# Performance work log

Hardware: AMD Instinct MI355X
Metric: run time of the kernel (lower is better)

## Reference

```python
import jax, jax.numpy as jnp
import numpy as np

H = 16        # num attention heads
KVH = 4       # num key/value heads
D = 128       # head dim
WIN = 1024    # sliding window (in packed per-state positions)
THETA = 10000.0
NUM_STATES = 8


def rotate_half(x):
    half = x.shape[-1] // 2
    return jnp.concatenate([-x[..., half:], x[..., :half]], axis=-1)


def setup_inputs() -> dict:
    key = jax.random.key(0)
    ks = jax.random.split(key, 6)
    B, L, HID = 2, 2048, 2048
    s = 0.02
    hidden_states = jax.random.normal(ks[0], (B, L, HID), jnp.float32)
    Wq = jax.random.normal(ks[1], (H * D, HID), jnp.float32) * s
    Wk = jax.random.normal(ks[2], (KVH * D, HID), jnp.float32) * s
    Wv = jax.random.normal(ks[3], (KVH * D, HID), jnp.float32) * s
    Wo = jax.random.normal(ks[4], (HID, H * D), jnp.float32) * s
    sid = jax.random.randint(ks[5], (B, L), 0, NUM_STATES).astype(jnp.int64)
    position_ids = jnp.tile(jnp.arange(L, dtype=jnp.int64)[None, :], (B, 1))
    return dict(hidden_states=hidden_states, Wq=Wq, Wk=Wk, Wv=Wv, Wo=Wo,
                sid=sid, position_ids=position_ids)


def reference(hidden_states, Wq, Wk, Wv, Wo, sid, position_ids):
    B, L, HID = hidden_states.shape
    # projections (Linear without bias: x @ W.T)
    q = (hidden_states @ Wq.T).reshape(B, L, H, D)
    k = (hidden_states @ Wk.T).reshape(B, L, KVH, D)
    v = (hidden_states @ Wv.T).reshape(B, L, KVH, D)
    # rotary embedding
    inv_freq = 1.0 / (THETA ** (jnp.arange(0, D, 2, dtype=jnp.float32) / D))
    freqs = position_ids.astype(jnp.float32)[:, :, None] * inv_freq[None, None, :]  # [B,L,D/2]
    emb = jnp.concatenate([freqs, freqs], axis=-1)                                  # [B,L,D]
    cos = jnp.cos(emb)[:, :, None, :].astype(hidden_states.dtype)
    sin = jnp.sin(emb)[:, :, None, :].astype(hidden_states.dtype)
    q = q * cos + rotate_half(q) * sin
    k = k * cos + rotate_half(k) * sin
    # GQA: repeat kv heads (repeat_interleave along head dim)
    n_rep = H // KVH
    k = jnp.repeat(k, n_rep, axis=2)  # [B,L,H,D]
    v = jnp.repeat(v, n_rep, axis=2)
    # BoSs mask: attend within same state id, causal, sliding window over
    # packed-per-state rank distance (equivalent to the varlen packing path)
    same = sid[:, :, None] == sid[:, None, :]                  # [B,L,L]
    tril = jnp.tril(jnp.ones((L, L), dtype=bool))[None]        # [1,L,L]
    rank = jnp.sum(same & tril, axis=-1) - 1                   # [B,L] rank within own state
    win_ok = (rank[:, :, None] - rank[:, None, :]) <= WIN
    mask = same & tril & win_ok                                # [B,L,L]
    scale = D ** -0.5
    scores = jnp.einsum('bqhd,bkhd->bhqk', q, k) * scale       # [B,H,L,L]
    scores = jnp.where(mask[:, None, :, :], scores, jnp.finfo(scores.dtype).min)
    attn = jax.nn.softmax(scores, axis=-1)
    o = jnp.einsum('bhqk,bkhd->bqhd', attn, v).reshape(B, L, H * D)
    return o @ Wo.T
```

## Files before the change

kernel.cpp:

```cpp
#include <hip/hip_runtime.h>
#include <hip/hip_bf16.h>

#define H_ 16
#define KVH_ 4
#define D_ 128
#define L_ 2048
#define B_ 2
#define HID_ 2048
#define WIN_ 1024
#define NS_ 8
#define QKV_N 3072

typedef __attribute__((ext_vector_type(8))) short short8;
typedef __attribute__((ext_vector_type(4))) float floatx4;

__device__ inline float bf16_to_f(unsigned short u) {
    union { unsigned int i; float f; } c; c.i = ((unsigned int)u) << 16; return c.f;
}
__device__ inline unsigned short f_to_bf16(float f) {
    __hip_bfloat16 h = __float2bfloat16(f);
    return *(unsigned short*)&h;
}

__device__ inline int world_is_bf16(const unsigned short* hs_u) {
    int lane = threadIdx.x & 63;
    unsigned short u = hs_u[(lane & 31) * 2];
    int e = (u >> 7) & 0xFF;
    unsigned long long bad = __ballot(e > 130);
    return bad == 0ULL;
}
__device__ inline int pid_stride(const int* pids) { return (pids[1] == 0) ? 2 : 1; }

__global__ __launch_bounds__(256) void convert_all(const void* __restrict__ hs,
                                                   const void* __restrict__ Wq,
                                                   const void* __restrict__ Wk,
                                                   const void* __restrict__ Wv,
                                                   const void* __restrict__ Wo,
                                                   unsigned short* __restrict__ c_hs,
                                                   unsigned short* __restrict__ c_Wq,
                                                   unsigned short* __restrict__ c_Wk,
                                                   unsigned short* __restrict__ c_Wv,
                                                   unsigned short* __restrict__ c_Wo) {
    int isbf = world_is_bf16((const unsigned short*)hs);
    const int N0 = (B_ * L_ * HID_) / 4;
    const int N1 = (HID_ * HID_) / 4;
    const int N2 = (KVH_ * D_ * HID_) / 4;
    const int N3 = N2;
    const int N4 = N1;
    const int total = N0 + N1 + N2 + N3 + N4;
    for (int i = blockIdx.x * 256 + threadIdx.x; i < total; i += gridDim.x * 256) {
        int j = i;
        const void* src; unsigned short* dst;
        if (j < N0)              { src = hs; dst = c_hs; }
        else if ((j -= N0) < N1) { src = Wq; dst = c_Wq; }
        else if ((j -= N1) < N2) { src = Wk; dst = c_Wk; }
        else if ((j -= N2) < N3) { src = Wv; dst = c_Wv; }
        else                     { j -= N3; src = Wo; dst = c_Wo; }
        if (isbf) {
            ((ushort4*)dst)[j] = ((const ushort4*)src)[j];
        } else {
            float4 f = ((const float4*)src)[j];
            ushort4 o4;
            o4.x = f_to_bf16(f.x); o4.y = f_to_bf16(f.y);
            o4.z = f_to_bf16(f.z); o4.w = f_to_bf16(f.w);
            ((ushort4*)dst)[j] = o4;
        }
    }
}

__global__ __launch_bounds__(256) void scan_kernel(const int* __restrict__ sid,
                                                   const int* __restrict__ pids,
                                                   int* __restrict__ rank,
                                                   int* __restrict__ poslist,
                                                   int* __restrict__ counts) {
    int stride = pid_stride(pids);
    int b = blockIdx.x;
    int t = threadIdx.x;
    __shared__ int cnt[256][NS_];
    __shared__ int pre[256][NS_];
    const int* s = sid + (size_t)b * L_ * stride;
    int myid[8];
#pragma unroll
    for (int i = 0; i < 8; i++) myid[i] = s[(t * 8 + i) * stride];
#pragma unroll
    for (int st = 0; st < NS_; st++) cnt[t][st] = 0;
#pragma unroll
    for (int i = 0; i < 8; i++) cnt[t][myid[i]]++;
    __syncthreads();
    for (int off = 1; off < 256; off <<= 1) {
        int add[NS_];
        if (t >= off)
#pragma unroll
            for (int st = 0; st < NS_; st++) add[st] = cnt[t - off][st];
        __syncthreads();
        if (t >= off)
#pragma unroll
            for (int st = 0; st < NS_; st++) cnt[t][st] += add[st];
        __syncthreads();
    }
#pragma unroll
    for (int st = 0; st < NS_; st++) pre[t][st] = t ? cnt[t - 1][st] : 0;
    if (t == 255)
#pragma unroll
        for (int st = 0; st < NS_; st++) counts[b * NS_ + st] = cnt[255][st];
    __syncthreads();
#pragma unroll
    for (int i = 0; i < 8; i++) {
        int sd = myid[i];
        int r = pre[t][sd]++;
        int pos = t * 8 + i;
        rank[b * L_ + pos] = r;
        poslist[((size_t)b * NS_ + sd) * L_ + r] = pos;
    }
}

#define STAGE(gptr, ldsdst)                                                     \
    __builtin_amdgcn_global_load_lds(                                           \
        (const __attribute__((address_space(1))) unsigned int*)(gptr),          \
        (__attribute__((address_space(3))) unsigned int*)(ldsdst), 16, 0, 0)

#define SB __builtin_amdgcn_sched_barrier(0)

#define RD_A(dst, MH, KK)                                                       \
    _Pragma("unroll")                                                           \
    for (int mt = 0; mt < MT; ++mt)                                             \
        dst[mt] = *(const short8*)&Ab[(arow + (MH) * (MT * 16) + mt * 16) * 64  \
                                      + ((((KK) << 2) | quad) ^ axor) * 8]

#define RD_B(dst, KK)                                                           \
    _Pragma("unroll")                                                           \
    for (int nt = 0; nt < 4; ++nt)                                              \
        dst[nt] = *(const short8*)&Bb[(brr + nt * 16) * 64                      \
                                      + ((((KK) << 2) | quad) ^ axor) * 8]

#define MFMA_C(AV, BV, MH)                                                      \
    __builtin_amdgcn_s_setprio(1);                                              \
    _Pragma("unroll")                                                           \
    for (int mt = 0; mt < MT; ++mt)                                             \
        _Pragma("unroll")                                                       \
        for (int nt = 0; nt < 4; ++nt)                                          \
            acc[(MH) * MT + mt][nt] = __builtin_amdgcn_mfma_f32_16x16x32_bf16(  \
                AV[mt], BV[nt], acc[(MH) * MT + mt][nt], 0, 0, 0);              \
    __builtin_amdgcn_s_setprio(0)

template<int MT>
__global__ __launch_bounds__(512, 1) void gemm_t(const unsigned short* __restrict__ A,
                                                 const unsigned short* __restrict__ B0,
                                                 const unsigned short* __restrict__ B1,
                                                 const unsigned short* __restrict__ B2,
                                                 void* __restrict__ C,
                                                 int M, int N, int K,
                                                 int nb1, int nb2,
                                                 const unsigned short* __restrict__ hs_probe,
                                                 int c_mode) {
    __shared__ unsigned short As[2][MT * 4096];
    __shared__ unsigned short Bs[2][16384];
    int tid = threadIdx.x;
    int wave = tid >> 6, lane = tid & 63;
    int quad = lane >> 4, l16 = lane & 15;
    int wr = wave >> 2, wc = wave & 3;
    int bn_t = blockIdx.x;
    int bm = blockIdx.y * (MT * 64), bn = bn_t * 256;

    const unsigned short* Bseg;
    int brow0;
    if (bn_t < nb1)      { Bseg = B0; brow0 = bn; }
    else if (bn_t < nb2) { Bseg = B1; brow0 = bn - nb1 * 256; }
    else                 { Bseg = B2; brow0 = bn - nb2 * 256; }

    int sub = tid >> 3, slot = tid & 7;
    int swz = slot ^ (sub & 7);
    unsigned int a_off[MT], b_off[4];
#pragma unroll
    for (int c = 0; c < MT; ++c)
        a_off[c] = (unsigned int)((bm + c * 64 + sub) * K + swz * 8);
#pragma unroll
    for (int c = 0; c < 4; ++c)
        b_off[c] = (unsigned int)((brow0 + c * 64 + sub) * K + swz * 8);

    const int arow = wr * (MT * 32) + l16;
    const int brr  = wc * 64 + l16;
    const int axor = l16 & 7;

    floatx4 acc[2 * MT][4] = {};
    short8 a0[MT], a1[MT], b0[4], b1[4];
    const int KT = K >> 6;

#pragma unroll
    for (int c = 0; c < 4; ++c)  STAGE(Bseg + b_off[c], &Bs[0][c * 4096 + tid * 8]);
#pragma unroll
    for (int c = 0; c < MT; ++c) STAGE(A + a_off[c], &As[0][c * 4096 + tid * 8]);

    for (int t = 0; t < KT; ++t) {
        const unsigned short* Ab = As[t & 1];
        const unsigned short* Bb = Bs[t & 1];
        unsigned short* AsN = As[(t & 1) ^ 1];
        unsigned short* BsN = Bs[(t & 1) ^ 1];
        int tn = (t + 1 < KT) ? t + 1 : t;
        unsigned int kel = (unsigned int)tn * 64;

        asm volatile("s_waitcnt vmcnt(0)" ::: "memory");
        __builtin_amdgcn_s_barrier();
        asm volatile("" ::: "memory");

        RD_A(a0, 0, 0);
        RD_B(b0, 0);
        RD_A(a1, 1, 0);
#pragma unroll
        for (int c = 0; c < 4; ++c)
            STAGE(Bseg + b_off[c] + kel, &BsN[c * 4096 + tid * 8]);
        SB;
        MFMA_C(a0, b0, 0);
        SB;
        RD_A(a0, 0, 1);
        RD_B(b1, 1);
#pragma unroll
        for (int c = 0; c < MT; ++c)
            STAGE(A + a_off[c] + kel, &AsN[c * 4096 + tid * 8]);
        SB;
        MFMA_C(a1, b0, 1);
        SB;
        RD_A(a1, 1, 1);
        SB;
        MFMA_C(a0, b1, 0);
        SB;
        MFMA_C(a1, b1, 1);
    }
    asm volatile("s_waitcnt vmcnt(0)" ::: "memory");

    int cf32 = c_mode ? !world_is_bf16(hs_probe) : 0;
#pragma unroll
    for (int a = 0; a < 2 * MT; ++a)
#pragma unroll
        for (int g = 0; g < 4; ++g)
#pragma unroll
            for (int r = 0; r < 4; ++r) {
                int row = bm + wr * (MT * 32) + (a / MT) * (MT * 16)
                        + (a % MT) * 16 + quad * 4 + r;
                int col = bn + wc * 64 + g * 16 + l16;
                size_t idx = (size_t)row * N + col;
                if (cf32) ((float*)C)[idx] = acc[a][g][r];
                else      ((unsigned short*)C)[idx] = f_to_bf16(acc[a][g][r]);
            }
}

__global__ __launch_bounds__(256) void rope_kernel(unsigned short* __restrict__ qkv,
                                                   const int* __restrict__ pos_ids) {
    int stride = pid_stride(pos_ids);
    int idx = blockIdx.x * 256 + threadIdx.x;
    int i = idx & 63;
    int tmp = idx >> 6;
    int head = tmp % 20;
    int bl = tmp / 20;
    if (bl >= B_ * L_) return;
    float posf = (float)pos_ids[bl * stride];
    float inv = exp2f(-(float)i * (2.0f / 128.0f) * 13.287712379549449f);
    float ang = posf * inv;
    float c = cosf(ang), sn = sinf(ang);
    unsigned short* p = qkv + (size_t)bl * QKV_N +
                        ((head < H_) ? head * D_ : 2048 + (head - H_) * D_);
    float x0 = bf16_to_f(p[i]), x1 = bf16_to_f(p[i + 64]);
    p[i]      = f_to_bf16(x0 * c - x1 * sn);
    p[i + 64] = f_to_bf16(x1 * c + x0 * sn);
}

__global__ __launch_bounds__(256, 4) void attn_mfma(const unsigned short* __restrict__ qkv,
                                                    const int* __restrict__ counts,
                                                    const int* __restrict__ poslist,
                                                    unsigned short* __restrict__ o) {
    int qt  = blockIdx.x & 127;
    int kvh = (blockIdx.x >> 7) & 3;
    int s   = (blockIdx.x >> 9) & 7;
    int b   = blockIdx.x >> 12;
    int n = counts[b * NS_ + s];
    if (qt * 16 >= n) return;
    const int* plist = poslist + ((size_t)b * NS_ + s) * L_;

    __shared__ short Ksh[32][136];
    __shared__ short Vsh[128][40];
    __shared__ short Psh[4][16][40];
    __shared__ int posq[16];

    int tid = threadIdx.x;
    int wave = tid >> 6, lane = tid & 63;
    int quad = lane >> 4, l16 = lane & 15;
    int h = kvh * 4 + wave;
    const float scale = 0.08838834764831845f;

    if (tid < 16) posq[tid] = plist[min(qt * 16 + tid, n - 1)];
    __syncthreads();

    short8 qf[4];
    {
        const unsigned short* gq =
            qkv + ((size_t)(b << 11) + posq[l16]) * QKV_N + h * D_;
#pragma unroll
        for (int kk = 0; kk < 4; kk++)
            qf[kk] = *(const short8*)(gq + kk * 32 + quad * 8);
    }

    float m_r[4], l_r[4];
    floatx4 Ov[8];
#pragma unroll
    for (int r4 = 0; r4 < 4; r4++) { m_r[r4] = -1e30f; l_r[r4] = 0.f; }
#pragma unroll
    for (int nt = 0; nt < 8; nt++) Ov[nt] = (floatx4){0.f, 0.f, 0.f, 0.f};

    int c0 = max(0, (qt * 16 - WIN_) >> 5);
    int nch = ((qt * 16 + 15) >> 5) + 1;

    int r = tid >> 3, seg = tid & 7;
    int vc = r ^ ((seg & 3) << 3);
    short8 kr0, kr1, vr0, vr1;
    {
        int kpos = plist[min(c0 * 32 + r, n - 1)];
        size_t base = ((size_t)(b << 11) + kpos) * QKV_N + 2048 + kvh * D_ + seg * 16;
        kr0 = *(const short8*)(qkv + base);
        kr1 = *(const short8*)(qkv + base + 8);
        vr0 = *(const short8*)(qkv + base + 512);
        vr1 = *(const short8*)(qkv + base + 520);
    }

    for (int c = c0; c < nch; c++) {
        *(short8*)&Ksh[r][seg * 16]     = kr0;
        *(short8*)&Ksh[r][seg * 16 + 8] = kr1;
#pragma unroll
        for (int e = 0; e < 8; e++) Vsh[seg * 16 + e][vc] = vr0[e];
#pragma unroll
        for (int e = 0; e < 8; e++) Vsh[seg * 16 + 8 + e][vc] = vr1[e];
        __syncthreads();

        if (c + 1 < nch) {
            int kpos = plist[min((c + 1) * 32 + r, n - 1)];
            size_t base = ((size_t)(b << 11) + kpos) * QKV_N + 2048 + kvh * D_ + seg * 16;
            kr0 = *(const short8*)(qkv + base);
            kr1 = *(const short8*)(qkv + base + 8);
            vr0 = *(const short8*)(qkv + base + 512);
            vr1 = *(const short8*)(qkv + base + 520);
        }

        floatx4 s0 = (floatx4){0.f, 0.f, 0.f, 0.f};
        floatx4 s1 = (floatx4){0.f, 0.f, 0.f, 0.f};
#pragma unroll
        for (int kk = 0; kk < 4; kk++) {
            short8 kfa = *(const short8*)&Ksh[l16][kk * 32 + quad * 8];
            s0 = __builtin_amdgcn_mfma_f32_16x16x32_bf16(qf[kk], kfa, s0, 0, 0, 0);
        }
#pragma unroll
        for (int kk = 0; kk < 4; kk++) {
            short8 kfb = *(const short8*)&Ksh[16 + l16][kk * 32 + quad * 8];
            s1 = __builtin_amdgcn_mfma_f32_16x16x32_bf16(qf[kk], kfb, s1, 0, 0, 0);
        }

        int kr0i = c * 32 + l16, kr1i = kr0i + 16;
        float x0[4], x1[4], rmax[4];
#pragma unroll
        for (int r4 = 0; r4 < 4; r4++) {
            int qr = qt * 16 + quad * 4 + r4;
            bool mk0 = (kr0i <= qr) && (kr0i >= qr - WIN_);
            bool mk1 = (kr1i <= qr) && (kr1i >= qr - WIN_);
            x0[r4] = mk0 ? s0[r4] * scale : -1e30f;
            x1[r4] = mk1 ? s1[r4] * scale : -1e30f;
            rmax[r4] = fmaxf(x0[r4], x1[r4]);
        }
#pragma unroll
        for (int st = 1; st <= 8; st <<= 1)
#pragma unroll
            for (int r4 = 0; r4 < 4; r4++)
                rmax[r4] = fmaxf(rmax[r4], __shfl_xor(rmax[r4], st, 64));
        float al[4], psum[4];
#pragma unroll
        for (int r4 = 0; r4 < 4; r4++) {
            float nm = fmaxf(m_r[r4], rmax[r4]);
            al[r4] = __expf(m_r[r4] - nm);
            m_r[r4] = nm;
            x0[r4] = (x0[r4] > -1e29f) ? __expf(x0[r4] - nm) : 0.f;
            x1[r4] = (x1[r4] > -1e29f) ? __expf(x1[r4] - nm) : 0.f;
            psum[r4] = x0[r4] + x1[r4];
        }
#pragma unroll
        for (int st = 1; st <= 8; st <<= 1)
#pragma unroll
            for (int r4 = 0; r4 < 4; r4++)
                psum[r4] += __shfl_xor(psum[r4], st, 64);
#pragma unroll
        for (int r4 = 0; r4 < 4; r4++) l_r[r4] = l_r[r4] * al[r4] + psum[r4];
#pragma unroll
        for (int nt = 0; nt < 8; nt++)
#pragma unroll
            for (int r4 = 0; r4 < 4; r4++) Ov[nt][r4] *= al[r4];

#pragma unroll
        for (int r4 = 0; r4 < 4; r4++) {
            Psh[wave][quad * 4 + r4][l16]      = (short)f_to_bf16(x0[r4]);
            Psh[wave][quad * 4 + r4][16 + l16] = (short)f_to_bf16(x1[r4]);
        }
        short8 pf = *(const short8*)&Psh[wave][l16][quad * 8];

#pragma unroll
        for (int nt = 0; nt < 8; nt++) {
            short8 vf = *(const short8*)&Vsh[nt * 16 + l16][(quad ^ (nt & 3)) * 8];
            Ov[nt] = __builtin_amdgcn_mfma_f32_16x16x32_bf16(pf, vf, Ov[nt], 0, 0, 0);
        }
        __syncthreads();
    }

    float inv_r[4];
    int pos_r[4], qvalid[4];
#pragma unroll
    for (int r4 = 0; r4 < 4; r4++) {
        int qr = qt * 16 + quad * 4 + r4;
        qvalid[r4] = (qr < n);
        inv_r[r4] = 1.f / l_r[r4];
        pos_r[r4] = posq[quad * 4 + r4];
    }
#pragma unroll
    for (int nt = 0; nt < 8; nt++)
#pragma unroll
        for (int r4 = 0; r4 < 4; r4++)
            if (qvalid[r4])
                o[(((size_t)(b << 11) + pos_r[r4]) * H_ + h) * D_ + nt * 16 + l16] =
                    f_to_bf16(Ov[nt][r4] * inv_r[r4]);
}

extern "C" void kernel_launch(void* const* d_in, const int* in_sizes, int n_in,
                              void* d_out, int out_size, void* d_ws, size_t ws_size,
                              hipStream_t stream) {
    const void* hs = d_in[0];
    const void* Wq = d_in[1];
    const void* Wk = d_in[2];
    const void* Wv = d_in[3];
    const void* Wo = d_in[4];
    const int* sid  = (const int*)d_in[5];
    const int* pids = (const int*)d_in[6];

    const int M = B_ * L_;
    char* w = (char*)d_ws;
    unsigned short* qkv  = (unsigned short*)(w + 256);
    unsigned short* o_b  = (unsigned short*)(w + 25166080);
    unsigned short* c_hs = (unsigned short*)(w + 41943296);
    unsigned short* c_Wq = (unsigned short*)(w + 58720512);
    unsigned short* c_Wk = (unsigned short*)(w + 67109120);
    unsigned short* c_Wv = (unsigned short*)(w + 69206272);
    unsigned short* c_Wo = (unsigned short*)(w + 71303424);
    int* rank            = (int*)(w + 79692032);
    int* plist           = (int*)(w + 79708416);
    int* counts          = (int*)(w + 79839488);

    const unsigned short* hs_probe = (const unsigned short*)hs;

    convert_all<<<2048, 256, 0, stream>>>(hs, Wq, Wk, Wv, Wo,
                                          c_hs, c_Wq, c_Wk, c_Wv, c_Wo);

    scan_kernel<<<B_, 256, 0, stream>>>(sid, pids, rank, plist, counts);

    gemm_t<4><<<dim3(QKV_N / 256, M / 256), 512, 0, stream>>>(
        c_hs, c_Wq, c_Wk, c_Wv, qkv, M, QKV_N, HID_, 8, 10, hs_probe, 0);

    int rope_threads = M * (H_ + KVH_) * 64;
    rope_kernel<<<(rope_threads + 255) / 256, 256, 0, stream>>>(qkv, pids);

    attn_mfma<<<B_ * NS_ * KVH_ * (L_ / 16), 256, 0, stream>>>(qkv, counts, plist, o_b);

    gemm_t<2><<<dim3(HID_ / 256, M / 128), 512, 0, stream>>>(
        o_b, c_Wo, c_Wo, c_Wo, d_out, M, HID_, HID_, 1 << 30, 1 << 30, hs_probe, 1);
}
```

Before: 300.3 us.

## Deepen GEMM pipeline to four-stage LDS ring with K=32 tiles

The projection GEMM's K-step shrinks from 64 to 32, and the double-buffered LDS is replaced by a 4-slot ring with 3 tiles prefetched ahead. The full vmcnt(0) wait becomes a partial vmcnt wait, so loads stay in flight across iterations. The LDS swizzle changes to a 4-slot XOR pattern and all fragments are read up front before the MFMAs. The aim is to hide global latency better, at the cost of twice as many barriers per K and a different bank-conflict pattern.

```diff
diff --git a/kernel.cpp b/kernel.cpp
--- a/kernel.cpp
+++ b/kernel.cpp
@@ -121,26 +121,14 @@
 
 #define SB __builtin_amdgcn_sched_barrier(0)
 
-#define RD_A(dst, MH, KK)                                                       \
-    _Pragma("unroll")                                                           \
-    for (int mt = 0; mt < MT; ++mt)                                             \
-        dst[mt] = *(const short8*)&Ab[(arow + (MH) * (MT * 16) + mt * 16) * 64  \
-                                      + ((((KK) << 2) | quad) ^ axor) * 8]
-
-#define RD_B(dst, KK)                                                           \
-    _Pragma("unroll")                                                           \
-    for (int nt = 0; nt < 4; ++nt)                                              \
-        dst[nt] = *(const short8*)&Bb[(brr + nt * 16) * 64                      \
-                                      + ((((KK) << 2) | quad) ^ axor) * 8]
-
-#define MFMA_C(AV, BV, MH)                                                      \
+#define MFMA_P(P)                                                               \
     __builtin_amdgcn_s_setprio(1);                                              \
     _Pragma("unroll")                                                           \
-    for (int mt = 0; mt < MT; ++mt)                                             \
+    for (int m2 = 0; m2 < 2; ++m2)                                              \
         _Pragma("unroll")                                                       \
         for (int nt = 0; nt < 4; ++nt)                                          \
-            acc[(MH) * MT + mt][nt] = __builtin_amdgcn_mfma_f32_16x16x32_bf16(  \
-                AV[mt], BV[nt], acc[(MH) * MT + mt][nt], 0, 0, 0);              \
+            acc[(P) * 2 + m2][nt] = __builtin_amdgcn_mfma_f32_16x16x32_bf16(    \
+                fA[(P) * 2 + m2], fB[nt], acc[(P) * 2 + m2][nt], 0, 0, 0);      \
     __builtin_amdgcn_s_setprio(0)
 
 template<int MT>
@@ -153,8 +141,9 @@
                                                  int nb1, int nb2,
                                                  const unsigned short* __restrict__ hs_probe,
                                                  int c_mode) {
-    __shared__ unsigned short As[2][MT * 4096];
-    __shared__ unsigned short Bs[2][16384];
+    const int CH_A = MT / 2;
+    __shared__ unsigned short As[4][MT * 2048];
+    __shared__ unsigned short Bs[4][8192];
     int tid = threadIdx.x;
     int wave = tid >> 6, lane = tid & 63;
     int quad = lane >> 4, l16 = lane & 15;
@@ -168,63 +157,68 @@
     else if (bn_t < nb2) { Bseg = B1; brow0 = bn - nb1 * 256; }
     else                 { Bseg = B2; brow0 = bn - nb2 * 256; }
 
-    int sub = tid >> 3, slot = tid & 7;
-    int swz = slot ^ (sub & 7);
-    unsigned int a_off[MT], b_off[4];
-#pragma unroll
-    for (int c = 0; c < MT; ++c)
-        a_off[c] = (unsigned int)((bm + c * 64 + sub) * K + swz * 8);
-#pragma unroll
-    for (int c = 0; c < 4; ++c)
-        b_off[c] = (unsigned int)((brow0 + c * 64 + sub) * K + swz * 8);
+    int sub = tid >> 2, slot = tid & 3;
+    int swz = slot ^ ((sub >> 1) & 3);
+    unsigned int a_off[CH_A], b_off[2];
+#pragma unroll
+    for (int c = 0; c < CH_A; ++c)
+        a_off[c] = (unsigned int)((bm + c * 128 + sub) * K + swz * 8);
+#pragma unroll
+    for (int c = 0; c < 2; ++c)
+        b_off[c] = (unsigned int)((brow0 + c * 128 + sub) * K + swz * 8);
 
     const int arow = wr * (MT * 32) + l16;
     const int brr  = wc * 64 + l16;
-    const int axor = l16 & 7;
+    const int xr   = (l16 >> 1) & 3;
 
     floatx4 acc[2 * MT][4] = {};
-    short8 a0[MT], a1[MT], b0[4], b1[4];
-    const int KT = K >> 6;
-
-#pragma unroll
-    for (int c = 0; c < 4; ++c)  STAGE(Bseg + b_off[c], &Bs[0][c * 4096 + tid * 8]);
-#pragma unroll
-    for (int c = 0; c < MT; ++c) STAGE(A + a_off[c], &As[0][c * 4096 + tid * 8]);
+    short8 fA[2 * MT], fB[4];
+    const int KT = K >> 5;
+
+#pragma unroll
+    for (int pt = 0; pt < 3; ++pt) {
+        unsigned int kel = (unsigned int)pt * 32;
+#pragma unroll
+        for (int c = 0; c < 2; ++c)
+            STAGE(Bseg + b_off[c] + kel, &Bs[pt][c * 4096 + tid * 8]);
+#pragma unroll
+        for (int c = 0; c < CH_A; ++c)
+            STAGE(A + a_off[c] + kel, &As[pt][c * 4096 + tid * 8]);
+    }
 
     for (int t = 0; t < KT; ++t) {
-        const unsigned short* Ab = As[t & 1];
-        const unsigned short* Bb = Bs[t & 1];
-        unsigned short* AsN = As[(t & 1) ^ 1];
-        unsigned short* BsN = Bs[(t & 1) ^ 1];
-        int tn = (t + 1 < KT) ? t + 1 : t;
-        unsigned int kel = (unsigned int)tn * 64;
-
-        asm volatile("s_waitcnt vmcnt(0)" ::: "memory");
+        const unsigned short* Ab = As[t & 3];
+        const unsigned short* Bb = Bs[t & 3];
+        int nbuf = (t + 3) & 3;
+        int t3 = (t + 3 < KT) ? t + 3 : KT - 1;
+        unsigned int kel = (unsigned int)t3 * 32;
+
+        if constexpr (MT == 4) asm volatile("s_waitcnt vmcnt(8)" ::: "memory");
+        else                   asm volatile("s_waitcnt vmcnt(6)" ::: "memory");
         __builtin_amdgcn_s_barrier();
         asm volatile("" ::: "memory");
 
-        RD_A(a0, 0, 0);
-        RD_B(b0, 0);
-        RD_A(a1, 1, 0);
-#pragma unroll
-        for (int c = 0; c < 4; ++c)
-            STAGE(Bseg + b_off[c] + kel, &BsN[c * 4096 + tid * 8]);
+#pragma unroll
+        for (int nt = 0; nt < 4; ++nt)
+            fB[nt] = *(const short8*)&Bb[(brr + nt * 16) * 32 + ((quad ^ xr) * 8)];
+#pragma unroll
+        for (int mt = 0; mt < 2 * MT; ++mt)
+            fA[mt] = *(const short8*)&Ab[(arow + mt * 16) * 32 + ((quad ^ xr) * 8)];
         SB;
-        MFMA_C(a0, b0, 0);
+
+#pragma unroll
+        for (int c = 0; c < 2; ++c)
+            STAGE(Bseg + b_off[c] + kel, &Bs[nbuf][c * 4096 + tid * 8]);
+#pragma unroll
+        for (int c = 0; c < CH_A; ++c)
+            STAGE(A + a_off[c] + kel, &As[nbuf][c * 4096 + tid * 8]);
         SB;
-        RD_A(a0, 0, 1);
-        RD_B(b1, 1);
-#pragma unroll
-        for (int c = 0; c < MT; ++c)
-            STAGE(A + a_off[c] + kel, &AsN[c * 4096 + tid * 8]);
-        SB;
-        MFMA_C(a1, b0, 1);
-        SB;
-        RD_A(a1, 1, 1);
-        SB;
-        MFMA_C(a0, b1, 0);
-        SB;
-        MFMA_C(a1, b1, 1);
+
+        MFMA_P(0); SB;
+        MFMA_P(1);
+        if constexpr (MT == 4) {
+            SB; MFMA_P(2); SB; MFMA_P(3);
+        }
     }
     asm volatile("s_waitcnt vmcnt(0)" ::: "memory");
 
@@ -235,8 +229,7 @@
         for (int g = 0; g < 4; ++g)
 #pragma unroll
             for (int r = 0; r < 4; ++r) {
-                int row = bm + wr * (MT * 32) + (a / MT) * (MT * 16)
-                        + (a % MT) * 16 + quad * 4 + r;
+                int row = bm + wr * (MT * 32) + a * 16 + quad * 4 + r;
                 int col = bn + wc * 64 + g * 16 + l16;
                 size_t idx = (size_t)row * N + col;
                 if (cf32) ((float*)C)[idx] = acc[a][g][r];
```

New measurement: 295.1 us. No clear change (-1.7%).
